# Kernel tuning notes

Measured on AMD Instinct MI355X. Metric: run time of the kernel, lower is better.

Reference implementation:

```python
import jax, jax.numpy as jnp
import numpy as np

B, S, D, H = 4, 1024, 1024, 16
DEPTH = D // H


def setup_inputs() -> dict:
    key = jax.random.key(0)
    ks = jax.random.split(key, 12)
    scale = 1.0 / np.sqrt(D)
    return {
        "query": jax.random.normal(ks[0], (B, S, D), jnp.float32),
        "key_in": jax.random.normal(ks[1], (B, S, D), jnp.float32),
        "value": jax.random.normal(ks[2], (B, S, D), jnp.float32),
        "mask": jnp.zeros((B, 1, 1, S), jnp.float32),
        "wq": jax.random.normal(ks[3], (D, D), jnp.float32) * scale,
        "bq": jnp.zeros((D,), jnp.float32),
        "wk": jax.random.normal(ks[4], (D, D), jnp.float32) * scale,
        "bk": jnp.zeros((D,), jnp.float32),
        "wv": jax.random.normal(ks[5], (D, D), jnp.float32) * scale,
        "bv": jnp.zeros((D,), jnp.float32),
        "wo": jax.random.normal(ks[6], (D, D), jnp.float32) * scale,
        "bo": jnp.zeros((D,), jnp.float32),
    }


def _split_heads(x):
    b, s, _ = x.shape
    return x.reshape(b, s, H, DEPTH).transpose(0, 2, 1, 3)  # [B,H,S,depth]


def reference(query, key_in, value, mask, wq, bq, wk, bk, wv, bv, wo, bo):
    q = _split_heads(query @ wq + bq)
    k = _split_heads(key_in @ wk + bk)
    v = _split_heads(value @ wv + bv)
    # scaled dot-product attention, full O(S^2) scores as in the original
    scores = jnp.einsum("bhqd,bhkd->bhqk", q, k) / jnp.sqrt(jnp.float32(DEPTH))
    scores = scores + mask * (-1e9)
    attn = jax.nn.softmax(scores, axis=-1)
    ctx = jnp.einsum("bhqk,bhkd->bhqd", attn, v)
    concat = ctx.transpose(0, 2, 1, 3).reshape(query.shape[0], -1, D)
    return concat @ wo + bo
```

## Files before the change

### kernel.cpp

```cpp
#include <hip/hip_runtime.h>
#include <hip/hip_bf16.h>
#include <stdint.h>

#define B_ 4
#define S_ 1024
#define D_ 1024
#define H_ 16
#define DEPTH_ 64

typedef __attribute__((ext_vector_type(8))) short bf16x8;
typedef __attribute__((ext_vector_type(4))) float f32x4;
typedef unsigned short ubf16;

#define BAR() do { asm volatile("" ::: "memory"); __builtin_amdgcn_s_barrier(); asm volatile("" ::: "memory"); } while (0)

__device__ __forceinline__ ubf16 f2bf(float f) {
  union { float f; unsigned u; } v; v.f = f;
  unsigned r = v.u + 0x7fffu + ((v.u >> 16) & 1u);
  return (ubf16)(r >> 16);
}

__device__ __forceinline__ void async16(void* lds, const void* g) {
  __builtin_amdgcn_global_load_lds(
      (const __attribute__((address_space(1))) void*)g,
      (__attribute__((address_space(3))) void*)lds, 16, 0, 0);
}

struct Tp4 { const float* W[4]; ubf16* WT[4]; };
__global__ __launch_bounds__(256) void transpose4_bf16(Tp4 a) {
  __shared__ float tile[32][33];
  const float* W = a.W[blockIdx.z];
  ubf16* WT = a.WT[blockIdx.z];
  int n0 = blockIdx.x * 32, k0 = blockIdx.y * 32;
  int tx = threadIdx.x & 31, ty = threadIdx.x >> 5;
#pragma unroll
  for (int i = 0; i < 4; ++i)
    tile[ty + i * 8][tx] = W[(size_t)(k0 + ty + i * 8) * D_ + n0 + tx];
  __syncthreads();
#pragma unroll
  for (int i = 0; i < 4; ++i)
    WT[(size_t)(n0 + ty + i * 8) * D_ + k0 + tx] = f2bf(tile[tx][ty + i * 8]);
}

struct GemmUnitF {
  const float* A; const ubf16* BT; const float* bias; void* out; int mode;
};
struct GemmArgsF { GemmUnitF u[3]; };

__global__ __launch_bounds__(256) void gemm_qkv_fused(GemmArgsF args) {
  const GemmUnitF gu = args.u[blockIdx.z];
  const int orig = blockIdx.x + (blockIdx.y << 3);
  const int xcd = orig & 7, j = orig >> 3;
  const int bm0 = (xcd * 4 + (j & 3)) * 128;
  const int bn0 = (j >> 2) * 128;
  const int tid = threadIdx.x, wid = tid >> 6, lane = tid & 63;
  const int wr = wid >> 1, wc = wid & 1;
  const int l15 = lane & 15, l4 = lane >> 4;
  const int K = 1024;

  __shared__ __align__(16) ubf16 As[2][128 * 32];
  __shared__ __align__(16) ubf16 Bs[2][128 * 32];
  f32x4 acc[4][4] = {};

  int cc0, cc1;
  const float* aP0; const float* aP1;
  const ubf16* bP0; const ubf16* bP1;
  {
    cc0 = tid;           int r0 = cc0 >> 2, s0 = cc0 & 3, g0 = s0 ^ ((r0 >> 1) & 3);
    cc1 = 256 + tid;     int r1 = cc1 >> 2, s1 = cc1 & 3, g1 = s1 ^ ((r1 >> 1) & 3);
    aP0 = gu.A + (size_t)(bm0 + r0) * K + g0 * 8;
    aP1 = gu.A + (size_t)(bm0 + r1) * K + g1 * 8;
    bP0 = gu.BT + (size_t)(bn0 + r0) * K + g0 * 8;
    bP1 = gu.BT + (size_t)(bn0 + r1) * K + g1 * 8;
  }
  int aOff[4], bOff[4];
#pragma unroll
  for (int f = 0; f < 4; ++f) {
    int ra = wr * 64 + f * 16 + l15;
    aOff[f] = ra * 64 + (l4 ^ ((ra >> 1) & 3)) * 16;
    int rb = wc * 64 + f * 16 + l15;
    bOff[f] = rb * 64 + (l4 ^ ((rb >> 1) & 3)) * 16;
  }

  {
    async16((char*)&Bs[0][0] + wid * 1024, bP0); bP0 += 32;
    async16((char*)&Bs[0][0] + 4096 + wid * 1024, bP1); bP1 += 32;
    f32x4 a00 = *(const f32x4*)aP0, a01 = *(const f32x4*)(aP0 + 4); aP0 += 32;
    f32x4 a10 = *(const f32x4*)aP1, a11 = *(const f32x4*)(aP1 + 4); aP1 += 32;
    bf16x8 w0, w1;
#pragma unroll
    for (int q = 0; q < 4; ++q) {
      w0[q] = (short)f2bf(a00[q]); w0[4 + q] = (short)f2bf(a01[q]);
      w1[q] = (short)f2bf(a10[q]); w1[4 + q] = (short)f2bf(a11[q]);
    }
    *(bf16x8*)((char*)&As[0][0] + cc0 * 16) = w0;
    *(bf16x8*)((char*)&As[0][0] + cc1 * 16) = w1;
    asm volatile("s_waitcnt vmcnt(0) lgkmcnt(0)" ::: "memory");
  }
  BAR();

#pragma unroll 1
  for (int t = 0; t < 31; ++t) {
    const int cur = t & 1;
    async16((char*)&Bs[cur ^ 1][0] + wid * 1024, bP0); bP0 += 32;
    async16((char*)&Bs[cur ^ 1][0] + 4096 + wid * 1024, bP1); bP1 += 32;
    f32x4 a00 = *(const f32x4*)aP0, a01 = *(const f32x4*)(aP0 + 4); aP0 += 32;
    f32x4 a10 = *(const f32x4*)aP1, a11 = *(const f32x4*)(aP1 + 4); aP1 += 32;
    __builtin_amdgcn_sched_barrier(0);
    bf16x8 af[4], bfr[4];
#pragma unroll
    for (int mi = 0; mi < 4; ++mi)
      af[mi] = *(const bf16x8*)((const char*)&As[cur][0] + aOff[mi]);
#pragma unroll
    for (int ni = 0; ni < 4; ++ni)
      bfr[ni] = *(const bf16x8*)((const char*)&Bs[cur][0] + bOff[ni]);
#pragma unroll
    for (int mi = 0; mi < 4; ++mi)
#pragma unroll
      for (int ni = 0; ni < 4; ++ni)
        acc[mi][ni] = __builtin_amdgcn_mfma_f32_16x16x32_bf16(af[mi], bfr[ni], acc[mi][ni], 0, 0, 0);
    __builtin_amdgcn_sched_barrier(0);
    bf16x8 w0, w1;
#pragma unroll
    for (int q = 0; q < 4; ++q) {
      w0[q] = (short)f2bf(a00[q]); w0[4 + q] = (short)f2bf(a01[q]);
      w1[q] = (short)f2bf(a10[q]); w1[4 + q] = (short)f2bf(a11[q]);
    }
    *(bf16x8*)((char*)&As[cur ^ 1][0] + cc0 * 16) = w0;
    *(bf16x8*)((char*)&As[cur ^ 1][0] + cc1 * 16) = w1;
    asm volatile("s_waitcnt vmcnt(0) lgkmcnt(0)" ::: "memory");
    BAR();
  }
  {
    bf16x8 af[4], bfr[4];
#pragma unroll
    for (int mi = 0; mi < 4; ++mi)
      af[mi] = *(const bf16x8*)((const char*)&As[1][0] + aOff[mi]);
#pragma unroll
    for (int ni = 0; ni < 4; ++ni)
      bfr[ni] = *(const bf16x8*)((const char*)&Bs[1][0] + bOff[ni]);
#pragma unroll
    for (int mi = 0; mi < 4; ++mi)
#pragma unroll
      for (int ni = 0; ni < 4; ++ni)
        acc[mi][ni] = __builtin_amdgcn_mfma_f32_16x16x32_bf16(af[mi], bfr[ni], acc[mi][ni], 0, 0, 0);
  }

  float bv[4];
#pragma unroll
  for (int ni = 0; ni < 4; ++ni) bv[ni] = gu.bias[bn0 + wc * 64 + ni * 16 + l15];
#pragma unroll
  for (int mi = 0; mi < 4; ++mi) {
#pragma unroll
    for (int ni = 0; ni < 4; ++ni) {
#pragma unroll
      for (int r = 0; r < 4; ++r) {
        int m = bm0 + wr * 64 + mi * 16 + l4 * 4 + r;
        int n = bn0 + wc * 64 + ni * 16 + l15;
        float v = acc[mi][ni][r] + bv[ni];
        if (gu.mode == 0) {
          ((ubf16*)gu.out)[(size_t)m * 1024 + n] = f2bf(v);
        } else {
          int b = m >> 10, s = m & 1023, h = n >> 6, d = n & 63;
          ((ubf16*)gu.out)[(((size_t)(b * H_ + h)) * DEPTH_ + d) * S_ + s] = f2bf(v);
        }
      }
    }
  }
}

struct GemmUnit {
  const ubf16* A; const ubf16* BT; const float* bias; void* out; int mode;
};
struct GemmArgs { GemmUnit u[3]; };

__global__ __launch_bounds__(256) void gemm_bt(GemmArgs args, int M, int N) {
  const GemmUnit gu = args.u[blockIdx.z];
  const int orig = blockIdx.x + (blockIdx.y << 3);
  const int xcd = orig & 7, j = orig >> 3;
  const int bm0 = (xcd * 4 + (j & 3)) * 128;
  const int bn0 = (j >> 2) * 128;
  const int tid = threadIdx.x, wid = tid >> 6, lane = tid & 63;
  const int wr = wid >> 1, wc = wid & 1;
  const int l15 = lane & 15, l4 = lane >> 4;
  const int K = 1024;

  __shared__ __align__(16) ubf16 As[2][128 * 32];
  __shared__ __align__(16) ubf16 Bs[2][128 * 32];
  f32x4 acc[4][4] = {};

  const ubf16* aCur[2]; const ubf16* bCur[2];
#pragma unroll
  for (int i = 0; i < 2; ++i) {
    int c = i * 256 + tid;
    int r = c >> 2, s = c & 3;
    int cg = s ^ ((r >> 1) & 3);
    aCur[i] = gu.A + (size_t)(bm0 + r) * K + cg * 8;
    bCur[i] = gu.BT + (size_t)(bn0 + r) * K + cg * 8;
  }
  auto stageAdv = [&](int bf) {
#pragma unroll
    for (int i = 0; i < 2; ++i) {
      async16((char*)&As[bf][0] + i * 4096 + wid * 1024, aCur[i]);
      async16((char*)&Bs[bf][0] + i * 4096 + wid * 1024, bCur[i]);
      aCur[i] += 32; bCur[i] += 32;
    }
  };
  int aOff[4], bOff[4];
#pragma unroll
  for (int f = 0; f < 4; ++f) {
    int ra = wr * 64 + f * 16 + l15;
    aOff[f] = ra * 64 + (l4 ^ ((ra >> 1) & 3)) * 16;
    int rb = wc * 64 + f * 16 + l15;
    bOff[f] = rb * 64 + (l4 ^ ((rb >> 1) & 3)) * 16;
  }

  stageAdv(0);
  for (int t = 0; t < 32; ++t) {
    const int cur = t & 1;
    if (t < 31) {
      stageAdv(cur ^ 1);
      asm volatile("s_waitcnt vmcnt(4)" ::: "memory");
    } else {
      asm volatile("s_waitcnt vmcnt(0)" ::: "memory");
    }
    BAR();
    bf16x8 af[4], bfr[4];
#pragma unroll
    for (int mi = 0; mi < 4; ++mi)
      af[mi] = *(const bf16x8*)((const char*)&As[cur][0] + aOff[mi]);
#pragma unroll
    for (int ni = 0; ni < 4; ++ni)
      bfr[ni] = *(const bf16x8*)((const char*)&Bs[cur][0] + bOff[ni]);
#pragma unroll
    for (int mi = 0; mi < 4; ++mi)
#pragma unroll
      for (int ni = 0; ni < 4; ++ni)
        acc[mi][ni] = __builtin_amdgcn_mfma_f32_16x16x32_bf16(af[mi], bfr[ni], acc[mi][ni], 0, 0, 0);
    BAR();
  }

  float bv[4];
#pragma unroll
  for (int ni = 0; ni < 4; ++ni) bv[ni] = gu.bias[bn0 + wc * 64 + ni * 16 + l15];
#pragma unroll
  for (int mi = 0; mi < 4; ++mi) {
#pragma unroll
    for (int ni = 0; ni < 4; ++ni) {
#pragma unroll
      for (int r = 0; r < 4; ++r) {
        int m = bm0 + wr * 64 + mi * 16 + l4 * 4 + r;
        int n = bn0 + wc * 64 + ni * 16 + l15;
        float v = acc[mi][ni][r] + bv[ni];
        if (gu.mode == 0) {
          ((ubf16*)gu.out)[(size_t)m * N + n] = f2bf(v);
        } else if (gu.mode == 1) {
          int b = m >> 10, s = m & 1023, h = n >> 6, d = n & 63;
          ((ubf16*)gu.out)[(((size_t)(b * H_ + h)) * DEPTH_ + d) * S_ + s] = f2bf(v);
        } else {
          ((float*)gu.out)[(size_t)m * N + n] = v;
        }
      }
    }
  }
}

__global__ __launch_bounds__(256) void attention_fwd(
    const ubf16* __restrict__ Q, const ubf16* __restrict__ Kg,
    const ubf16* __restrict__ VT, const float* __restrict__ mask,
    ubf16* __restrict__ ctx) {
  const int lid = blockIdx.y * 8 + blockIdx.x;
  const int t0 = (lid & 7) * 64 + (lid >> 3);
  const int qt = t0 & 7, bh = t0 >> 3;
  const int b = bh >> 4, h = bh & 15;
  const int tid = threadIdx.x, wid = tid >> 6, lane = tid & 63;
  const int l15 = lane & 15, l4 = lane >> 4;
  const int q0 = qt * 128 + wid * 32;

  __shared__ __align__(16) ubf16 Ks[2][4096];
  __shared__ __align__(16) ubf16 Vs[2][4096];
  __shared__ __align__(16) ubf16 Ps[4][32][72];

  const ubf16* kb = Kg + ((size_t)(b * S_)) * D_ + h * DEPTH_;
  const ubf16* vb = VT + ((size_t)bh) * DEPTH_ * S_;

  bf16x8 aq[2][2];
#pragma unroll
  for (int mi = 0; mi < 2; ++mi)
#pragma unroll
    for (int kk = 0; kk < 2; ++kk)
      aq[mi][kk] = *(const bf16x8*)&Q[((size_t)(b * S_ + q0 + mi * 16 + l15)) * D_ +
                                      h * DEPTH_ + kk * 32 + l4 * 8];

  bf16x8 ones;
#pragma unroll
  for (int j = 0; j < 8; ++j) ones[j] = (short)0x3F80;

  f32x4 cacc[2][4] = {};
  f32x4 csum[2] = {};

  const float* mrow = mask + b * S_;
  const float C1 = 0.125f * 1.44269504f;
  const float CM = -1.0e9f * 1.44269504f;

  auto stage = [&](int bf, int kt) {
#pragma unroll
    for (int i = 0; i < 2; ++i) {
      int c = i * 256 + tid;
      int r = c >> 3, cg = (c & 7) ^ (r & 7);
      async16((char*)&Ks[bf][0] + i * 4096 + wid * 1024,
              kb + (size_t)(kt + r) * D_ + cg * 8);
      async16((char*)&Vs[bf][0] + i * 4096 + wid * 1024,
              vb + (size_t)r * S_ + kt + cg * 8);
    }
  };

  stage(0, 0);
  __syncthreads();

  for (int t = 0; t < 16; ++t) {
    const int cur = t & 1;
    const int kt = t * 64;
    if (t < 15) stage(cur ^ 1, kt + 64);

    bf16x8 kf[4][2];
#pragma unroll
    for (int nf = 0; nf < 4; ++nf)
#pragma unroll
      for (int kk = 0; kk < 2; ++kk) {
        int kr = nf * 16 + l15;
        int c16 = (kk * 4 + l4) ^ (kr & 7);
        kf[nf][kk] = *(const bf16x8*)((const char*)&Ks[cur][0] + kr * 128 + c16 * 16);
      }
    bf16x8 vf[4][2];
#pragma unroll
    for (int df = 0; df < 4; ++df)
#pragma unroll
      for (int kk = 0; kk < 2; ++kk) {
        int dr = df * 16 + l15;
        int c16 = (kk * 4 + l4) ^ (dr & 7);
        vf[df][kk] = *(const bf16x8*)((const char*)&Vs[cur][0] + dr * 128 + c16 * 16);
      }

    f32x4 sc[2][4];
#pragma unroll
    for (int mi = 0; mi < 2; ++mi)
#pragma unroll
      for (int nf = 0; nf < 4; ++nf) {
        f32x4 z = {0.f, 0.f, 0.f, 0.f};
        z = __builtin_amdgcn_mfma_f32_16x16x32_bf16(aq[mi][0], kf[nf][0], z, 0, 0, 0);
        z = __builtin_amdgcn_mfma_f32_16x16x32_bf16(aq[mi][1], kf[nf][1], z, 0, 0, 0);
        sc[mi][nf] = z;
      }

    float mvl[4];
#pragma unroll
    for (int nf = 0; nf < 4; ++nf) mvl[nf] = mrow[kt + nf * 16 + l15] * CM;

#pragma unroll
    for (int mi = 0; mi < 2; ++mi)
#pragma unroll
      for (int nf = 0; nf < 4; ++nf)
#pragma unroll
        for (int r = 0; r < 4; ++r) {
          float p = __builtin_amdgcn_exp2f(fmaf(sc[mi][nf][r], C1, mvl[nf]));
          Ps[wid][mi * 16 + l4 * 4 + r][nf * 16 + l15] = f2bf(p);
        }

    bf16x8 pf[2][2];
#pragma unroll
    for (int mi = 0; mi < 2; ++mi)
#pragma unroll
      for (int kk = 0; kk < 2; ++kk)
        pf[mi][kk] = *(const bf16x8*)&Ps[wid][mi * 16 + l15][kk * 32 + l4 * 8];

#pragma unroll
    for (int mi = 0; mi < 2; ++mi) {
#pragma unroll
      for (int df = 0; df < 4; ++df) {
        cacc[mi][df] = __builtin_amdgcn_mfma_f32_16x16x32_bf16(pf[mi][0], vf[df][0], cacc[mi][df], 0, 0, 0);
        cacc[mi][df] = __builtin_amdgcn_mfma_f32_16x16x32_bf16(pf[mi][1], vf[df][1], cacc[mi][df], 0, 0, 0);
      }
      csum[mi] = __builtin_amdgcn_mfma_f32_16x16x32_bf16(pf[mi][0], ones, csum[mi], 0, 0, 0);
      csum[mi] = __builtin_amdgcn_mfma_f32_16x16x32_bf16(pf[mi][1], ones, csum[mi], 0, 0, 0);
    }

    __syncthreads();
  }

#pragma unroll
  for (int mi = 0; mi < 2; ++mi) {
    float inv[4];
#pragma unroll
    for (int r = 0; r < 4; ++r) inv[r] = 1.0f / csum[mi][r];
#pragma unroll
    for (int df = 0; df < 4; ++df)
#pragma unroll
      for (int r = 0; r < 4; ++r) {
        int srow = q0 + mi * 16 + l4 * 4 + r;
        float v = cacc[mi][df][r] * inv[r];
        ctx[((size_t)(b * S_ + srow)) * D_ + h * DEPTH_ + df * 16 + l15] = f2bf(v);
      }
  }
}

extern "C" void kernel_launch(void* const* d_in, const int* in_sizes, int n_in,
                              void* d_out, int out_size, void* d_ws, size_t ws_size,
                              hipStream_t stream) {
  const float* query  = (const float*)d_in[0];
  const float* key_in = (const float*)d_in[1];
  const float* value  = (const float*)d_in[2];
  const float* mask   = (const float*)d_in[3];
  const float* wq = (const float*)d_in[4];
  const float* bq = (const float*)d_in[5];
  const float* wk = (const float*)d_in[6];
  const float* bk = (const float*)d_in[7];
  const float* wv = (const float*)d_in[8];
  const float* bv = (const float*)d_in[9];
  const float* wo = (const float*)d_in[10];
  const float* bo = (const float*)d_in[11];

  char* ws = (char*)d_ws;
  const size_t MB = 1024 * 1024;
  ubf16* WqT = (ubf16*)(ws + 24 * MB);
  ubf16* WkT = (ubf16*)(ws + 26 * MB);
  ubf16* WvT = (ubf16*)(ws + 28 * MB);
  ubf16* WoT = (ubf16*)(ws + 30 * MB);
  ubf16* Qb  = (ubf16*)(ws + 32 * MB);
  ubf16* Kb  = (ubf16*)(ws + 40 * MB);
  ubf16* VTb = (ubf16*)(ws + 48 * MB);
  ubf16* Ctx = (ubf16*)(ws + 56 * MB);

  Tp4 t4;
  t4.W[0] = wq; t4.WT[0] = WqT;
  t4.W[1] = wk; t4.WT[1] = WkT;
  t4.W[2] = wv; t4.WT[2] = WvT;
  t4.W[3] = wo; t4.WT[3] = WoT;
  transpose4_bf16<<<dim3(32, 32, 4), dim3(256), 0, stream>>>(t4);

  GemmArgsF g1;
  g1.u[0] = {query,  WqT, bq, (void*)Qb, 0};
  g1.u[1] = {key_in, WkT, bk, (void*)Kb, 0};
  g1.u[2] = {value,  WvT, bv, (void*)VTb, 1};
  gemm_qkv_fused<<<dim3(8, 32, 3), dim3(256), 0, stream>>>(g1);

  attention_fwd<<<dim3(8, 64), dim3(256), 0, stream>>>(Qb, Kb, VTb, mask, Ctx);

  GemmArgs g2;
  g2.u[0] = {Ctx, WoT, bo, d_out, 2};
  g2.u[1] = g2.u[0];
  g2.u[2] = g2.u[0];
  gemm_bt<<<dim3(8, 32, 1), dim3(256), 0, stream>>>(g2, 4096, 1024);
}
```

Before: 126.2 us.

## Load GEMM B operand directly into registers, bypassing LDS

Both projection GEMM kernels now stop staging the weight (B) tiles through shared memory. Each wave loads its B fragments straight from global memory into registers in MFMA layout, double-buffered across two register sets. The main loop is unrolled by two, and the wait counts are adjusted to the new mix of loads. This removes the B-side LDS writes, reads and footprint. In exchange, the two waves that share a column slice now load the same B data twice, the global accesses are less coalesced, and register pressure goes up.

```diff
diff --git a/kernel.cpp b/kernel.cpp
--- a/kernel.cpp
+++ b/kernel.cpp
@@ -59,92 +59,91 @@
   const int K = 1024;
 
   __shared__ __align__(16) ubf16 As[2][128 * 32];
-  __shared__ __align__(16) ubf16 Bs[2][128 * 32];
   f32x4 acc[4][4] = {};
 
   int cc0, cc1;
   const float* aP0; const float* aP1;
-  const ubf16* bP0; const ubf16* bP1;
   {
-    cc0 = tid;           int r0 = cc0 >> 2, s0 = cc0 & 3, g0 = s0 ^ ((r0 >> 1) & 3);
-    cc1 = 256 + tid;     int r1 = cc1 >> 2, s1 = cc1 & 3, g1 = s1 ^ ((r1 >> 1) & 3);
+    cc0 = tid;       int r0 = cc0 >> 2, s0 = cc0 & 3, g0 = s0 ^ ((r0 >> 1) & 3);
+    cc1 = 256 + tid; int r1 = cc1 >> 2, s1 = cc1 & 3, g1 = s1 ^ ((r1 >> 1) & 3);
     aP0 = gu.A + (size_t)(bm0 + r0) * K + g0 * 8;
     aP1 = gu.A + (size_t)(bm0 + r1) * K + g1 * 8;
-    bP0 = gu.BT + (size_t)(bn0 + r0) * K + g0 * 8;
-    bP1 = gu.BT + (size_t)(bn0 + r1) * K + g1 * 8;
-  }
-  int aOff[4], bOff[4];
+  }
+  const ubf16* bPtr0 = gu.BT + (size_t)(bn0 + wc * 64 + 0 * 16 + l15) * K + l4 * 8;
+  const ubf16* bPtr1 = gu.BT + (size_t)(bn0 + wc * 64 + 1 * 16 + l15) * K + l4 * 8;
+  const ubf16* bPtr2 = gu.BT + (size_t)(bn0 + wc * 64 + 2 * 16 + l15) * K + l4 * 8;
+  const ubf16* bPtr3 = gu.BT + (size_t)(bn0 + wc * 64 + 3 * 16 + l15) * K + l4 * 8;
+  int aOff[4];
 #pragma unroll
   for (int f = 0; f < 4; ++f) {
     int ra = wr * 64 + f * 16 + l15;
     aOff[f] = ra * 64 + (l4 ^ ((ra >> 1) & 3)) * 16;
-    int rb = wc * 64 + f * 16 + l15;
-    bOff[f] = rb * 64 + (l4 ^ ((rb >> 1) & 3)) * 16;
-  }
+  }
+
+  bf16x8 b0[4], b1[4];
+
+#define LOADB(DST) do { \
+    DST[0] = *(const bf16x8*)bPtr0; bPtr0 += 32; \
+    DST[1] = *(const bf16x8*)bPtr1; bPtr1 += 32; \
+    DST[2] = *(const bf16x8*)bPtr2; bPtr2 += 32; \
+    DST[3] = *(const bf16x8*)bPtr3; bPtr3 += 32; } while (0)
+
+#define LOADA() \
+    f32x4 a00 = *(const f32x4*)aP0, a01 = *(const f32x4*)(aP0 + 4); aP0 += 32; \
+    f32x4 a10 = *(const f32x4*)aP1, a11 = *(const f32x4*)(aP1 + 4); aP1 += 32;
+
+#define CVTWR(BUF) do { \
+    bf16x8 w0, w1; \
+    _Pragma("unroll") \
+    for (int q = 0; q < 4; ++q) { \
+      w0[q] = (short)f2bf(a00[q]); w0[4 + q] = (short)f2bf(a01[q]); \
+      w1[q] = (short)f2bf(a10[q]); w1[4 + q] = (short)f2bf(a11[q]); \
+    } \
+    *(bf16x8*)((char*)&As[BUF][0] + cc0 * 16) = w0; \
+    *(bf16x8*)((char*)&As[BUF][0] + cc1 * 16) = w1; } while (0)
+
+#define MFMAS(CUR, BC) do { \
+    bf16x8 af[4]; \
+    _Pragma("unroll") \
+    for (int mi = 0; mi < 4; ++mi) \
+      af[mi] = *(const bf16x8*)((const char*)&As[CUR][0] + aOff[mi]); \
+    _Pragma("unroll") \
+    for (int mi = 0; mi < 4; ++mi) \
+      _Pragma("unroll") \
+      for (int ni = 0; ni < 4; ++ni) \
+        acc[mi][ni] = __builtin_amdgcn_mfma_f32_16x16x32_bf16(af[mi], BC[ni], acc[mi][ni], 0, 0, 0); } while (0)
+
+#define BODY(CUR, BC, BN) do { \
+    LOADA(); \
+    LOADB(BN); \
+    __builtin_amdgcn_sched_barrier(0); \
+    MFMAS(CUR, BC); \
+    __builtin_amdgcn_sched_barrier(0); \
+    CVTWR(CUR ^ 1); \
+    asm volatile("s_waitcnt lgkmcnt(0)" ::: "memory"); \
+    __builtin_amdgcn_s_barrier(); \
+    asm volatile("" ::: "memory"); } while (0)
 
   {
-    async16((char*)&Bs[0][0] + wid * 1024, bP0); bP0 += 32;
-    async16((char*)&Bs[0][0] + 4096 + wid * 1024, bP1); bP1 += 32;
-    f32x4 a00 = *(const f32x4*)aP0, a01 = *(const f32x4*)(aP0 + 4); aP0 += 32;
-    f32x4 a10 = *(const f32x4*)aP1, a11 = *(const f32x4*)(aP1 + 4); aP1 += 32;
-    bf16x8 w0, w1;
-#pragma unroll
-    for (int q = 0; q < 4; ++q) {
-      w0[q] = (short)f2bf(a00[q]); w0[4 + q] = (short)f2bf(a01[q]);
-      w1[q] = (short)f2bf(a10[q]); w1[4 + q] = (short)f2bf(a11[q]);
-    }
-    *(bf16x8*)((char*)&As[0][0] + cc0 * 16) = w0;
-    *(bf16x8*)((char*)&As[0][0] + cc1 * 16) = w1;
-    asm volatile("s_waitcnt vmcnt(0) lgkmcnt(0)" ::: "memory");
-  }
-  BAR();
-
+    LOADA();
+    LOADB(b0);
+    CVTWR(0);
+    asm volatile("s_waitcnt lgkmcnt(0)" ::: "memory");
+    BAR();
+  }
 #pragma unroll 1
-  for (int t = 0; t < 31; ++t) {
-    const int cur = t & 1;
-    async16((char*)&Bs[cur ^ 1][0] + wid * 1024, bP0); bP0 += 32;
-    async16((char*)&Bs[cur ^ 1][0] + 4096 + wid * 1024, bP1); bP1 += 32;
-    f32x4 a00 = *(const f32x4*)aP0, a01 = *(const f32x4*)(aP0 + 4); aP0 += 32;
-    f32x4 a10 = *(const f32x4*)aP1, a11 = *(const f32x4*)(aP1 + 4); aP1 += 32;
-    __builtin_amdgcn_sched_barrier(0);
-    bf16x8 af[4], bfr[4];
-#pragma unroll
-    for (int mi = 0; mi < 4; ++mi)
-      af[mi] = *(const bf16x8*)((const char*)&As[cur][0] + aOff[mi]);
-#pragma unroll
-    for (int ni = 0; ni < 4; ++ni)
-      bfr[ni] = *(const bf16x8*)((const char*)&Bs[cur][0] + bOff[ni]);
-#pragma unroll
-    for (int mi = 0; mi < 4; ++mi)
-#pragma unroll
-      for (int ni = 0; ni < 4; ++ni)
-        acc[mi][ni] = __builtin_amdgcn_mfma_f32_16x16x32_bf16(af[mi], bfr[ni], acc[mi][ni], 0, 0, 0);
-    __builtin_amdgcn_sched_barrier(0);
-    bf16x8 w0, w1;
-#pragma unroll
-    for (int q = 0; q < 4; ++q) {
-      w0[q] = (short)f2bf(a00[q]); w0[4 + q] = (short)f2bf(a01[q]);
-      w1[q] = (short)f2bf(a10[q]); w1[4 + q] = (short)f2bf(a11[q]);
-    }
-    *(bf16x8*)((char*)&As[cur ^ 1][0] + cc0 * 16) = w0;
-    *(bf16x8*)((char*)&As[cur ^ 1][0] + cc1 * 16) = w1;
-    asm volatile("s_waitcnt vmcnt(0) lgkmcnt(0)" ::: "memory");
-    BAR();
-  }
-  {
-    bf16x8 af[4], bfr[4];
-#pragma unroll
-    for (int mi = 0; mi < 4; ++mi)
-      af[mi] = *(const bf16x8*)((const char*)&As[1][0] + aOff[mi]);
-#pragma unroll
-    for (int ni = 0; ni < 4; ++ni)
-      bfr[ni] = *(const bf16x8*)((const char*)&Bs[1][0] + bOff[ni]);
-#pragma unroll
-    for (int mi = 0; mi < 4; ++mi)
-#pragma unroll
-      for (int ni = 0; ni < 4; ++ni)
-        acc[mi][ni] = __builtin_amdgcn_mfma_f32_16x16x32_bf16(af[mi], bfr[ni], acc[mi][ni], 0, 0, 0);
-  }
+  for (int tt = 0; tt < 15; ++tt) {
+    BODY(0, b0, b1);
+    BODY(1, b1, b0);
+  }
+  BODY(0, b0, b1);
+  MFMAS(1, b1);
+
+#undef BODY
+#undef MFMAS
+#undef CVTWR
+#undef LOADA
+#undef LOADB
 
   float bv[4];
 #pragma unroll
@@ -186,59 +185,76 @@
   const int K = 1024;
 
   __shared__ __align__(16) ubf16 As[2][128 * 32];
-  __shared__ __align__(16) ubf16 Bs[2][128 * 32];
   f32x4 acc[4][4] = {};
 
-  const ubf16* aCur[2]; const ubf16* bCur[2];
+  const ubf16* aCur[2];
 #pragma unroll
   for (int i = 0; i < 2; ++i) {
     int c = i * 256 + tid;
     int r = c >> 2, s = c & 3;
     int cg = s ^ ((r >> 1) & 3);
     aCur[i] = gu.A + (size_t)(bm0 + r) * K + cg * 8;
-    bCur[i] = gu.BT + (size_t)(bn0 + r) * K + cg * 8;
-  }
-  auto stageAdv = [&](int bf) {
-#pragma unroll
-    for (int i = 0; i < 2; ++i) {
-      async16((char*)&As[bf][0] + i * 4096 + wid * 1024, aCur[i]);
-      async16((char*)&Bs[bf][0] + i * 4096 + wid * 1024, bCur[i]);
-      aCur[i] += 32; bCur[i] += 32;
-    }
-  };
-  int aOff[4], bOff[4];
+  }
+  const ubf16* bPtr0 = gu.BT + (size_t)(bn0 + wc * 64 + 0 * 16 + l15) * K + l4 * 8;
+  const ubf16* bPtr1 = gu.BT + (size_t)(bn0 + wc * 64 + 1 * 16 + l15) * K + l4 * 8;
+  const ubf16* bPtr2 = gu.BT + (size_t)(bn0 + wc * 64 + 2 * 16 + l15) * K + l4 * 8;
+  const ubf16* bPtr3 = gu.BT + (size_t)(bn0 + wc * 64 + 3 * 16 + l15) * K + l4 * 8;
+  int aOff[4];
 #pragma unroll
   for (int f = 0; f < 4; ++f) {
     int ra = wr * 64 + f * 16 + l15;
     aOff[f] = ra * 64 + (l4 ^ ((ra >> 1) & 3)) * 16;
-    int rb = wc * 64 + f * 16 + l15;
-    bOff[f] = rb * 64 + (l4 ^ ((rb >> 1) & 3)) * 16;
-  }
-
-  stageAdv(0);
-  for (int t = 0; t < 32; ++t) {
-    const int cur = t & 1;
-    if (t < 31) {
-      stageAdv(cur ^ 1);
-      asm volatile("s_waitcnt vmcnt(4)" ::: "memory");
-    } else {
-      asm volatile("s_waitcnt vmcnt(0)" ::: "memory");
-    }
-    BAR();
-    bf16x8 af[4], bfr[4];
-#pragma unroll
-    for (int mi = 0; mi < 4; ++mi)
-      af[mi] = *(const bf16x8*)((const char*)&As[cur][0] + aOff[mi]);
-#pragma unroll
-    for (int ni = 0; ni < 4; ++ni)
-      bfr[ni] = *(const bf16x8*)((const char*)&Bs[cur][0] + bOff[ni]);
-#pragma unroll
-    for (int mi = 0; mi < 4; ++mi)
-#pragma unroll
-      for (int ni = 0; ni < 4; ++ni)
-        acc[mi][ni] = __builtin_amdgcn_mfma_f32_16x16x32_bf16(af[mi], bfr[ni], acc[mi][ni], 0, 0, 0);
-    BAR();
-  }
+  }
+
+  bf16x8 b0[4], b1[4];
+
+#define LOADB(DST) do { \
+    DST[0] = *(const bf16x8*)bPtr0; bPtr0 += 32; \
+    DST[1] = *(const bf16x8*)bPtr1; bPtr1 += 32; \
+    DST[2] = *(const bf16x8*)bPtr2; bPtr2 += 32; \
+    DST[3] = *(const bf16x8*)bPtr3; bPtr3 += 32; } while (0)
+
+#define STAGEA(BUF) do { \
+    async16((char*)&As[BUF][0] + wid * 1024, aCur[0]); aCur[0] += 32; \
+    async16((char*)&As[BUF][0] + 4096 + wid * 1024, aCur[1]); aCur[1] += 32; } while (0)
+
+#define MFMAS(CUR, BC) do { \
+    bf16x8 af[4]; \
+    _Pragma("unroll") \
+    for (int mi = 0; mi < 4; ++mi) \
+      af[mi] = *(const bf16x8*)((const char*)&As[CUR][0] + aOff[mi]); \
+    _Pragma("unroll") \
+    for (int mi = 0; mi < 4; ++mi) \
+      _Pragma("unroll") \
+      for (int ni = 0; ni < 4; ++ni) \
+        acc[mi][ni] = __builtin_amdgcn_mfma_f32_16x16x32_bf16(af[mi], BC[ni], acc[mi][ni], 0, 0, 0); } while (0)
+
+#define BODY(CUR, BC, BN, LAST) do { \
+    if (!(LAST)) { STAGEA(CUR ^ 1); LOADB(BN); \
+      asm volatile("s_waitcnt vmcnt(6)" ::: "memory"); } \
+    else asm volatile("s_waitcnt vmcnt(0)" ::: "memory"); \
+    __builtin_amdgcn_s_barrier(); \
+    asm volatile("" ::: "memory"); \
+    __builtin_amdgcn_sched_barrier(0); \
+    MFMAS(CUR, BC); \
+    asm volatile("" ::: "memory"); \
+    __builtin_amdgcn_s_barrier(); \
+    asm volatile("" ::: "memory"); } while (0)
+
+  STAGEA(0);
+  LOADB(b0);
+#pragma unroll 1
+  for (int tt = 0; tt < 15; ++tt) {
+    BODY(0, b0, b1, false);
+    BODY(1, b1, b0, false);
+  }
+  BODY(0, b0, b1, false);
+  BODY(1, b1, b0, true);
+
+#undef BODY
+#undef MFMAS
+#undef STAGEA
+#undef LOADB
 
   float bv[4];
 #pragma unroll
```

Result: slower. 149.4 us (+18.4%).
